# Kernel tuning notes

Hardware: AMD Instinct MI355X
Metric: run time of the kernel (lower is better)

Reference implementation:

```python
import jax, jax.numpy as jnp
import numpy as np
from jax import lax

N_GROUPS = 2
TOPK_GROUPS = 1
TOPK = 4
ROUTE_SCALE = 1.0


def setup_inputs() -> dict:
    key = jax.random.key(0)
    k1, k2 = jax.random.split(key)
    T, D, E = 524288, 256, 64
    x = jax.random.normal(k1, (T, D), dtype=jnp.float32)
    W = jax.random.normal(k2, (E, D), dtype=jnp.float32) * 0.02  # router weight [out, in]
    return {"x": x, "W": W}


def reference(x, W):
    T = x.shape[0]
    E = W.shape[0]
    logits = x @ W.T  # [T, E]
    scores = jax.nn.softmax(logits.astype(jnp.float32), axis=-1)
    original_scores = scores
    # grouped masking (bias is None -> amax group score)
    g = scores.reshape(T, N_GROUPS, E // N_GROUPS)
    group_scores = g.max(axis=-1)  # [T, G]
    _, gidx = lax.top_k(group_scores, TOPK_GROUPS)  # [T, topk_groups]
    keep = jnp.zeros((T, N_GROUPS), dtype=bool).at[jnp.arange(T)[:, None], gidx].set(True)
    masked = jnp.where(keep[:, :, None], g, -jnp.inf).reshape(T, E)
    _, indices = lax.top_k(masked, TOPK)  # [T, topk]
    weights = jnp.take_along_axis(original_scores, indices, axis=1)
    weights = weights * ROUTE_SCALE
    return weights.astype(x.dtype), indices
```

## Files before the change

### kernel.cpp

```cpp
#include <hip/hip_runtime.h>
#include <hip/hip_bf16.h>
#include <stdint.h>


typedef __attribute__((ext_vector_type(8))) short bf16x8;
typedef __attribute__((ext_vector_type(4))) float f32x4;
typedef __attribute__((ext_vector_type(4))) int i32x4;

#define SPLIT_OFF 1024
#define LIST_OFF 102400
#define DELTA 1e-4f

__device__ __forceinline__ f32x4 mf(const i32x4& a, const i32x4& b,
                                    const f32x4& c) {
  return __builtin_amdgcn_mfma_f32_16x16x32_bf16(
      __builtin_bit_cast(bf16x8, a), __builtin_bit_cast(bf16x8, b), c, 0, 0, 0);
}

__device__ __forceinline__ int packhi(unsigned e0, unsigned e1) {
  return (int)__builtin_amdgcn_perm(e1, e0, 0x07060302u);
}

__device__ __forceinline__ void gload16(const void* g, void* l) {
  __builtin_amdgcn_global_load_lds(
      (const __attribute__((address_space(1))) void*)g,
      (__attribute__((address_space(3))) void*)l, 16, 0, 0);
}

__global__ void split_w(const float* __restrict__ W,
                        unsigned short* __restrict__ ws, int n,
                        int* __restrict__ meta) {
  int i = blockIdx.x * 256 + threadIdx.x;
  if (i == 0) meta[0] = 0;
  if (i >= n) return;
  float w = W[i];
  unsigned u = __float_as_uint(w);
  unsigned uh = u & 0xFFFF0000u;
  float rf = w - __uint_as_float(uh);
  unsigned short lv[2];
  lv[0] = (unsigned short)(uh >> 16);
  lv[1] = (unsigned short)(__float_as_uint(rf) >> 16);
  int e = i >> 8, k = i & 255;
  int nt = e >> 4, le = e & 15;
  int c = k >> 5, kc = k & 31;
  int half = kc >> 4, lg = (kc >> 2) & 3, pos = kc & 3;
  int kk = half * 4 + pos;
  int lane = lg * 16 + le;
#pragma unroll
  for (int v = 0; v < 2; ++v)
    ws[(((c * 8 + v * 4 + nt) * 64) + lane) * 8 + kk] = lv[v];
}

struct XF2 { i32x4 h, m; };

__device__ __forceinline__ XF2 split2(f32x4 a, f32x4 b) {
  float xs[8] = {a[0], a[1], a[2], a[3], b[0], b[1], b[2], b[3]};
  XF2 f;
#pragma unroll
  for (int wd = 0; wd < 4; ++wd) {
    unsigned u0 = __float_as_uint(xs[2 * wd]);
    unsigned u1 = __float_as_uint(xs[2 * wd + 1]);
    f.h[wd] = packhi(u0, u1);
    float r0 = xs[2 * wd] - __uint_as_float(u0 & 0xFFFF0000u);
    float r1 = xs[2 * wd + 1] - __uint_as_float(u1 & 0xFFFF0000u);
    f.m[wd] = packhi(__float_as_uint(r0), __float_as_uint(r1));
  }
  return f;
}

#define GL(dst, ptr, OFF)                                     \
  asm volatile("global_load_dwordx4 %0, %1, off offset:%2"    \
               : "=v"(dst)                                    \
               : "v"(ptr), "n"(OFF))

#define WAITV(NSTR)                                         \
  do {                                                      \
    asm volatile("s_waitcnt vmcnt(" NSTR ")" ::: "memory"); \
    __builtin_amdgcn_sched_barrier(0);                      \
  } while (0)

__global__ __launch_bounds__(512, 4) void gate_kernel(
    const float* __restrict__ x, const unsigned short* __restrict__ wsp,
    float* __restrict__ out, int* __restrict__ meta, int* __restrict__ list,
    int cap, int T) {
  __shared__ i32x4 WL[4096];

  const int t = threadIdx.x;
  const int lane = t & 63;
  const int wid = t >> 6;
  const int le = lane & 15;
  const int lg = lane >> 4;
  const int tokb = blockIdx.x * 256 + wid * 32;

  const float* xa0 = x + (size_t)(tokb + le) * 256 + lg * 4;
  const float* xa1 = xa0 + 16 * 256;

  f32x4 xbuf[2][4];
  f32x4 acc[4][2];
#pragma unroll
  for (int nt = 0; nt < 4; ++nt)
#pragma unroll
    for (int t2 = 0; t2 < 2; ++t2) acc[nt][t2] = (f32x4)0.0f;

#define STAGE_X(c)                              \
  do {                                          \
    GL(xbuf[(c) & 1][0], xa0, (c) * 128);       \
    GL(xbuf[(c) & 1][1], xa0, (c) * 128 + 64);  \
    GL(xbuf[(c) & 1][2], xa1, (c) * 128);       \
    GL(xbuf[(c) & 1][3], xa1, (c) * 128 + 64);  \
  } while (0)

#define ITER(c, NSTR)                                               \
  {                                                                 \
    WAITV(NSTR);                                                    \
    XF2 b0 = split2(xbuf[(c) & 1][0], xbuf[(c) & 1][1]);            \
    XF2 b1 = split2(xbuf[(c) & 1][2], xbuf[(c) & 1][3]);            \
    if ((c) + 2 < 8) STAGE_X((c) + 2);                              \
    _Pragma("unroll") for (int nt = 0; nt < 4; ++nt) {              \
      i32x4 ah = WL[(((c) * 8 + nt) << 6) + lane];                  \
      i32x4 am = WL[(((c) * 8 + 4 + nt) << 6) + lane];              \
      acc[nt][0] = mf(ah, b0.h, acc[nt][0]);                        \
      acc[nt][0] = mf(ah, b0.m, acc[nt][0]);                        \
      acc[nt][0] = mf(am, b0.h, acc[nt][0]);                        \
      acc[nt][0] = mf(am, b0.m, acc[nt][0]);                        \
      acc[nt][1] = mf(ah, b1.h, acc[nt][1]);                        \
      acc[nt][1] = mf(ah, b1.m, acc[nt][1]);                        \
      acc[nt][1] = mf(am, b1.h, acc[nt][1]);                        \
      acc[nt][1] = mf(am, b1.m, acc[nt][1]);                        \
    }                                                               \
  }

  {
    const char* wsrc = (const char*)wsp + t * 16;
    char* wdst = (char*)WL + t * 16;
#pragma unroll
    for (int i = 0; i < 8; ++i) gload16(wsrc + i * 8192, wdst + i * 8192);
  }
  STAGE_X(0);
  STAGE_X(1);
  WAITV("8");
  __builtin_amdgcn_s_barrier();

  ITER(0, "4");
  ITER(1, "4");
  ITER(2, "4");
  ITER(3, "4");
  ITER(4, "4");
  ITER(5, "4");
  ITER(6, "4");
  ITER(7, "0");

#pragma unroll
  for (int tt = 0; tt < 2; ++tt) {
    float l[16];
#pragma unroll
    for (int nt = 0; nt < 4; ++nt)
#pragma unroll
      for (int j = 0; j < 4; ++j) l[nt * 4 + j] = acc[nt][tt][j];

    float g0 = l[0], g1 = l[8];
#pragma unroll
    for (int j = 1; j < 8; ++j) {
      g0 = fmaxf(g0, l[j]);
      g1 = fmaxf(g1, l[8 + j]);
    }
    g0 = fmaxf(g0, __shfl_xor(g0, 16));
    g0 = fmaxf(g0, __shfl_xor(g0, 32));
    g1 = fmaxf(g1, __shfl_xor(g1, 16));
    g1 = fmaxf(g1, __shfl_xor(g1, 32));
    const int g = (g1 > g0) ? 1 : 0;
    const float m = fmaxf(g0, g1);

    float sum = 0.f;
#pragma unroll
    for (int k = 0; k < 16; ++k) sum += __expf(l[k] - m);
    sum += __shfl_xor(sum, 16);
    sum += __shfl_xor(sum, 32);
    const float inv = 1.0f / sum;

    float c[8];
    int ce[8];
#pragma unroll
    for (int j2 = 0; j2 < 8; ++j2) {
      c[j2] = l[g * 8 + j2];
      ce[j2] = (2 * g + (j2 >> 2)) * 16 + 4 * lg + (j2 & 3);
    }

    float v5[5];
    int e5[5];
#pragma unroll
    for (int it = 0; it < 5; ++it) {
      float bv = c[0];
      int be = ce[0];
#pragma unroll
      for (int j2 = 1; j2 < 8; ++j2) {
        bool gt = c[j2] > bv;
        bv = gt ? c[j2] : bv;
        be = gt ? ce[j2] : be;
      }
#pragma unroll
      for (int st = 0; st < 2; ++st) {
        int msk = 16 << st;
        float ov = __shfl_xor(bv, msk);
        int oe = __shfl_xor(be, msk);
        bool tk = (ov > bv) || (ov == bv && oe < be);
        bv = tk ? ov : bv;
        be = tk ? oe : be;
      }
      v5[it] = bv;
      e5[it] = be;
#pragma unroll
      for (int j2 = 0; j2 < 8; ++j2)
        c[j2] = (ce[j2] == be) ? -3.0e38f : c[j2];
    }

    float ming = fabsf(g0 - g1);
#pragma unroll
    for (int it = 0; it < 4; ++it) ming = fminf(ming, v5[it] - v5[it + 1]);

    if (lg == 0) {
      size_t trow = (size_t)tokb + tt * 16 + le;
      *(float4*)&out[trow * 4] =
          make_float4(__expf(v5[0] - m) * inv, __expf(v5[1] - m) * inv,
                      __expf(v5[2] - m) * inv, __expf(v5[3] - m) * inv);
      *(float4*)&out[(size_t)T * 4 + trow * 4] = make_float4(
          (float)e5[0], (float)e5[1], (float)e5[2], (float)e5[3]);
      if (ming < DELTA) {
        int p = atomicAdd(meta, 1);
        if (p < cap) list[p] = (int)trow;
      }
    }
  }
}

__global__ __launch_bounds__(64) void fix_kernel(
    const float* __restrict__ x, const float* __restrict__ W,
    float* __restrict__ out, const int* __restrict__ meta,
    const int* __restrict__ list, int cap, int T) {
  const int e = threadIdx.x;
  int cnt = meta[0];
  cnt = cnt < cap ? cnt : cap;
  for (int i = blockIdx.x; i < cnt; i += gridDim.x) {
    const int tok = list[i];
    const float* xr = x + (size_t)tok * 256;
    const float* wr = W + (size_t)e * 256;
    float acc = 0.f;
#pragma unroll 8
    for (int d = 0; d < 256; d += 4) {
      float4 xv = *(const float4*)(xr + d);
      float4 wv = *(const float4*)(wr + d);
      acc = fmaf(xv.x, wv.x, acc);
      acc = fmaf(xv.y, wv.y, acc);
      acc = fmaf(xv.z, wv.z, acc);
      acc = fmaf(xv.w, wv.w, acc);
    }
    float gm = acc;
#pragma unroll
    for (int st = 0; st < 5; ++st) gm = fmaxf(gm, __shfl_xor(gm, 1 << st));
    float om = __shfl_xor(gm, 32);
    float g0 = (e < 32) ? gm : om;
    float g1 = (e < 32) ? om : gm;
    const int g = (g1 > g0) ? 1 : 0;
    const float m = fmaxf(g0, g1);
    float sum = __expf(acc - m);
#pragma unroll
    for (int st = 0; st < 6; ++st) sum += __shfl_xor(sum, 1 << st);
    const float inv = 1.0f / sum;

    float cand = ((e >> 5) == g) ? acc : -3.0e38f;
    float w4[4], i4[4];
#pragma unroll
    for (int it = 0; it < 4; ++it) {
      float bv = cand;
      int be = e;
#pragma unroll
      for (int st = 0; st < 6; ++st) {
        int msk = 1 << st;
        float ov = __shfl_xor(bv, msk);
        int oe = __shfl_xor(be, msk);
        bool tk = (ov > bv) || (ov == bv && oe < be);
        bv = tk ? ov : bv;
        be = tk ? oe : be;
      }
      w4[it] = __expf(bv - m) * inv;
      i4[it] = (float)be;
      if (e == be) cand = -3.0e38f;
    }
    if (e == 0) {
      *(float4*)&out[(size_t)tok * 4] = make_float4(w4[0], w4[1], w4[2], w4[3]);
      *(float4*)&out[(size_t)T * 4 + (size_t)tok * 4] =
          make_float4(i4[0], i4[1], i4[2], i4[3]);
    }
  }
}

extern "C" void kernel_launch(void* const* d_in, const int* in_sizes, int n_in,
                              void* d_out, int out_size, void* d_ws,
                              size_t ws_size, hipStream_t stream) {
  const float* x = (const float*)d_in[0];
  const float* W = (const float*)d_in[1];
  float* out = (float*)d_out;
  int T = in_sizes[0] / 256;
  int nW = in_sizes[1];
  int* meta = (int*)d_ws;
  unsigned short* wsp = (unsigned short*)((char*)d_ws + SPLIT_OFF);
  int* list = (int*)((char*)d_ws + LIST_OFF);
  int cap = (ws_size > LIST_OFF + 4) ? (int)((ws_size - LIST_OFF) / 4) : 0;
  hipLaunchKernelGGL(split_w, dim3((nW + 255) / 256), dim3(256), 0, stream, W,
                     wsp, nW, meta);
  hipLaunchKernelGGL(gate_kernel, dim3(T / 256), dim3(512), 0, stream, x, wsp,
                     out, meta, list, cap, T);
  hipLaunchKernelGGL(fix_kernel, dim3(2048), dim3(64), 0, stream, x, W, out,
                     meta, list, cap, T);
}
```

Before: 142.0 us.

## Stage x tiles through swizzled LDS via global_load_lds instead of registers

```diff
diff --git a/kernel.cpp b/kernel.cpp
--- a/kernel.cpp
+++ b/kernel.cpp
@@ -68,22 +68,18 @@
   return f;
 }
 
-#define GL(dst, ptr, OFF)                                     \
-  asm volatile("global_load_dwordx4 %0, %1, off offset:%2"    \
-               : "=v"(dst)                                    \
-               : "v"(ptr), "n"(OFF))
-
 #define WAITV(NSTR)                                         \
   do {                                                      \
     asm volatile("s_waitcnt vmcnt(" NSTR ")" ::: "memory"); \
     __builtin_amdgcn_sched_barrier(0);                      \
   } while (0)
 
-__global__ __launch_bounds__(512, 4) void gate_kernel(
+__global__ __launch_bounds__(512, 2) void gate_kernel(
     const float* __restrict__ x, const unsigned short* __restrict__ wsp,
     float* __restrict__ out, int* __restrict__ meta, int* __restrict__ list,
     int cap, int T) {
   __shared__ i32x4 WL[4096];
+  __shared__ i32x4 XL[4096];
 
   const int t = threadIdx.x;
   const int lane = t & 63;
@@ -92,30 +88,50 @@
   const int lg = lane >> 4;
   const int tokb = blockIdx.x * 256 + wid * 32;
 
-  const float* xa0 = x + (size_t)(tokb + le) * 256 + lg * 4;
-  const float* xa1 = xa0 + 16 * 256;
-
-  f32x4 xbuf[2][4];
+  const int srow = lane >> 3;
+  const int spiece = (lane & 7) ^ srow;
+  const float* xg[4];
+#pragma unroll
+  for (int q = 0; q < 4; ++q)
+    xg[q] = x + (size_t)(tokb + q * 8 + srow) * 256 + spiece * 4;
+
+  char* XW = (char*)XL + wid * 8192;
+
+  const int s7 = le & 7;
+  const int abase = (le >> 3) * 1024 + s7 * 128;
+  const int o00 = abase + ((lg ^ s7) << 4);
+  const int o01 = abase + (((lg + 4) ^ s7) << 4);
+  const int o10 = o00 + 2048;
+  const int o11 = o01 + 2048;
+
   f32x4 acc[4][2];
 #pragma unroll
   for (int nt = 0; nt < 4; ++nt)
 #pragma unroll
     for (int t2 = 0; t2 < 2; ++t2) acc[nt][t2] = (f32x4)0.0f;
 
-#define STAGE_X(c)                              \
-  do {                                          \
-    GL(xbuf[(c) & 1][0], xa0, (c) * 128);       \
-    GL(xbuf[(c) & 1][1], xa0, (c) * 128 + 64);  \
-    GL(xbuf[(c) & 1][2], xa1, (c) * 128);       \
-    GL(xbuf[(c) & 1][3], xa1, (c) * 128 + 64);  \
+#define STAGE_X(c)                                                  \
+  do {                                                              \
+    char* xd_ = XW + (((c) & 1) << 12);                             \
+    gload16(xg[0] + (c) * 32, xd_);                                 \
+    gload16(xg[1] + (c) * 32, xd_ + 1024);                          \
+    gload16(xg[2] + (c) * 32, xd_ + 2048);                          \
+    gload16(xg[3] + (c) * 32, xd_ + 3072);                          \
   } while (0)
 
 #define ITER(c, NSTR)                                               \
   {                                                                 \
     WAITV(NSTR);                                                    \
-    XF2 b0 = split2(xbuf[(c) & 1][0], xbuf[(c) & 1][1]);            \
-    XF2 b1 = split2(xbuf[(c) & 1][2], xbuf[(c) & 1][3]);            \
+    const char* xb_ = XW + (((c) & 1) << 12);                       \
+    f32x4 r00 = *(const f32x4*)(xb_ + o00);                         \
+    f32x4 r01 = *(const f32x4*)(xb_ + o01);                         \
+    f32x4 r10 = *(const f32x4*)(xb_ + o10);                         \
+    f32x4 r11 = *(const f32x4*)(xb_ + o11);                         \
+    asm volatile("s_waitcnt lgkmcnt(0)" ::: "memory");              \
+    __builtin_amdgcn_sched_barrier(0);                              \
     if ((c) + 2 < 8) STAGE_X((c) + 2);                              \
+    XF2 b0 = split2(r00, r01);                                      \
+    XF2 b1 = split2(r10, r11);                                      \
     _Pragma("unroll") for (int nt = 0; nt < 4; ++nt) {              \
       i32x4 ah = WL[(((c) * 8 + nt) << 6) + lane];                  \
       i32x4 am = WL[(((c) * 8 + 4 + nt) << 6) + lane];              \
```

After: 170.8 us. +20.3%, slower.
